# Performance work log

Hardware: AMD Instinct MI355X
Metric: run time of the kernel (lower is better)

## Reference

```python
import jax, jax.numpy as jnp
import numpy as np

B, I, T, H, O = 256, 128, 256, 512, 2
EPS = 1e-5  # BatchNorm1d default eps


def setup_inputs() -> dict:
    key = jax.random.key(0)
    ks = jax.random.split(key, 32)
    stdv = 1.0 / np.sqrt(H)
    u = lambda k, shape: jax.random.uniform(k, shape, jnp.float32, -stdv, stdv)
    X = jax.random.normal(ks[0], (B, I, T), jnp.float32)
    Mask = (jax.random.uniform(ks[1], (B, I, T)) > 0.5).astype(jnp.float32)
    Delta = jax.random.uniform(ks[2], (B, I, T)) * 5.0
    inp = jnp.stack([X, Mask, Delta], axis=1)  # [B, 3, I, T]
    return dict(
        input=inp,
        x_mean=jnp.float32(0.0),
        W_dg_x=u(ks[3], (I, I)), b_dg_x=u(ks[4], (I,)),
        W_dg_h=u(ks[5], (I, H)), b_dg_h=u(ks[6], (H,)),
        W_xz=u(ks[7], (I, H)), W_hz=u(ks[8], (H, H)), W_mz=u(ks[9], (I, H)), b_z=u(ks[10], (H,)),
        W_xr=u(ks[11], (I, H)), W_hr=u(ks[12], (H, H)), W_mr=u(ks[13], (I, H)), b_r=u(ks[14], (H,)),
        W_xh=u(ks[15], (I, H)), W_hh=u(ks[16], (H, H)), W_mh=u(ks[17], (I, H)), b_h=u(ks[18], (H,)),
        W_hy=u(ks[19], (H, O)), b_hy=u(ks[20], (O,)),
        bn_gamma=u(ks[21], (H,)), bn_beta=u(ks[22], (H,)),
    )


def reference(input, x_mean, W_dg_x, b_dg_x, W_dg_h, b_dg_h,
              W_xz, W_hz, W_mz, b_z, W_xr, W_hr, W_mr, b_r,
              W_xh, W_hh, W_mh, b_h, W_hy, b_hy, bn_gamma, bn_beta):
    # input: [B, 3, I, T] -> time-major [T, B, I]
    Xs = jnp.transpose(input[:, 0], (2, 0, 1))
    Ms = jnp.transpose(input[:, 1], (2, 0, 1))
    Ds = jnp.transpose(input[:, 2], (2, 0, 1))
    b, i = input.shape[0], input.shape[2]
    h0 = jnp.zeros((b, W_hz.shape[0]), input.dtype)       # Hidden_State buffer (zeros, broadcast over batch)
    xl0 = jnp.zeros((b, i), input.dtype)                   # X_last_obs buffer

    def step(carry, xs):
        h, x_last = carry
        x, m, d = xs
        gamma_x = jnp.exp(-jax.nn.relu(d @ W_dg_x + b_dg_x))   # [B, I]
        gamma_h = jnp.exp(-jax.nn.relu(d @ W_dg_h + b_dg_h))   # [B, H]
        x_last = jnp.where(m > 0, x, x_last)
        x = m * x + (1 - m) * (gamma_x * x_last + (1 - gamma_x) * x_mean)
        h = gamma_h * h
        z = jax.nn.sigmoid(x @ W_xz + h @ W_hz + m @ W_mz + b_z)
        r = jax.nn.sigmoid(x @ W_xr + h @ W_hr + m @ W_mr + b_r)
        h_tilde = jnp.tanh(x @ W_xh + (r * h) @ W_hh + m @ W_mh + b_h)
        h = (1 - z) * h + z * h_tilde
        # BatchNorm1d in training mode: batch mean, biased variance
        mu = h.mean(axis=0)
        var = ((h - mu) ** 2).mean(axis=0)
        h = bn_gamma * (h - mu) * jax.lax.rsqrt(var + EPS) + bn_beta
        y = jax.nn.softplus(h @ W_hy + b_hy)
        return (h, x_last), (y, h)

    _, (ys, hs) = jax.lax.scan(step, (h0, xl0), (Xs, Ms, Ds))
    # back to batch-major [B, T, *]
    return jnp.transpose(ys, (1, 0, 2)), jnp.transpose(hs, (1, 0, 2))
```

## Files before the change

kernel.cpp:

```cpp
#include <hip/hip_runtime.h>
#include <math.h>

#define Bb 256
#define Ii 128
#define Tt 256
#define Hh 512
#define Oo 2
#define TBr (Tt*Bb)
#define EPS_BN 1e-5f

typedef __attribute__((ext_vector_type(8))) short short8;
typedef __attribute__((ext_vector_type(8))) __bf16 bf16x8;
typedef __attribute__((ext_vector_type(4))) float f32x4;
typedef unsigned long long u64;

__device__ __forceinline__ f32x4 mfma_bf16(short8 a, short8 b, f32x4 c) {
    return __builtin_amdgcn_mfma_f32_16x16x32_bf16(
        __builtin_bit_cast(bf16x8, a), __builtin_bit_cast(bf16x8, b), c, 0, 0, 0);
}
__device__ __forceinline__ short f2bf(float f) {
    union { float f; unsigned u; } v; v.f = f;
    unsigned r = (v.u + 0x7FFFu + ((v.u >> 16) & 1u)) >> 16;
    return (short)r;
}
__device__ __forceinline__ float bf2f(short s) {
    union { unsigned u; float f; } v; v.u = ((unsigned)(unsigned short)s) << 16;
    return v.f;
}
__device__ __forceinline__ float sigmoidf_(float x) { return 1.f / (1.f + expf(-x)); }
__device__ __forceinline__ float softplusf_(float x) { return fmaxf(x, 0.f) + log1pf(expf(-fabsf(x))); }

#define ALD_F(p)  __hip_atomic_load((p),  __ATOMIC_RELAXED, __HIP_MEMORY_SCOPE_AGENT)
#define AST_F(p,v) __hip_atomic_store((p), (v), __ATOMIC_RELAXED, __HIP_MEMORY_SCOPE_AGENT)
#define AADD_F(p,v) (void)__hip_atomic_fetch_add((p), (v), __ATOMIC_RELAXED, __HIP_MEMORY_SCOPE_AGENT)

__device__ __forceinline__ short8 ald16(const short* p) {
    union { u64 u[2]; short8 s; } v;
    v.u[0] = ALD_F((const u64*)p);
    v.u[1] = ALD_F((const u64*)(p + 4));
    return v.s;
}
__device__ __forceinline__ u64 pack4bf(float a, float b, float c_, float d) {
    return (u64)(unsigned short)f2bf(a)
         | ((u64)(unsigned short)f2bf(b) << 16)
         | ((u64)(unsigned short)f2bf(c_) << 32)
         | ((u64)(unsigned short)f2bf(d) << 48);
}

__global__ __launch_bounds__(1024) void repack_kernel(const float* __restrict__ in,
                                                      float* __restrict__ Xall,
                                                      short* __restrict__ Mall,
                                                      short* __restrict__ Dall)
{
    __shared__ float tile[32][33];
    const int bz = blockIdx.z;
    const int b = bz / 3, cch = bz % 3;
    const int t0 = blockIdx.x * 32, i0 = blockIdx.y * 32;
    const int tx = threadIdx.x, ty = threadIdx.y;
    const float* src = in + ((size_t)b * 3 + cch) * (size_t)Ii * Tt;
    tile[ty][tx] = src[(size_t)(i0 + ty) * Tt + t0 + tx];
    __syncthreads();
    const float v = tile[tx][ty];
    const size_t off = ((size_t)(t0 + ty) * Bb + b) * Ii + i0 + tx;
    if (cch == 0)      Xall[off] = v;
    else if (cch == 1) Mall[off] = f2bf(v);
    else               Dall[off] = f2bf(v);
}

__global__ __launch_bounds__(256) void pack_weights_kernel(
    const float* __restrict__ W_dg_x, const float* __restrict__ W_dg_h,
    const float* __restrict__ W_xz, const float* __restrict__ W_hz, const float* __restrict__ W_mz, const float* __restrict__ b_z,
    const float* __restrict__ W_xr, const float* __restrict__ W_hr, const float* __restrict__ W_mr, const float* __restrict__ b_r,
    const float* __restrict__ W_xh, const float* __restrict__ W_hh, const float* __restrict__ W_mh,
    short* __restrict__ Wc1T, short* __restrict__ Wc2T,
    short* __restrict__ WdgxT, short* __restrict__ WdghT, float* __restrict__ bias1)
{
    const int idx = blockIdx.x * blockDim.x + threadIdx.x;
    const int n1 = 1024 * 768, n2 = 512 * 768, n3 = 128 * 128, n4 = 512 * 128;
    if (idx < n1) {
        const int n = idx / 768, k = idx % 768;
        const int col = (n < Hh) ? n : (n - Hh);
        const float* Wx = (n < Hh) ? W_xz : W_xr;
        const float* Wm = (n < Hh) ? W_mz : W_mr;
        const float* Wh = (n < Hh) ? W_hz : W_hr;
        float v;
        if (k < Ii)        v = Wx[(size_t)k * Hh + col];
        else if (k < 2*Ii) v = Wm[(size_t)(k - Ii) * Hh + col];
        else               v = Wh[(size_t)(k - 2*Ii) * Hh + col];
        Wc1T[idx] = f2bf(v);
    } else if (idx < n1 + n2) {
        const int j = idx - n1;
        const int n = j / 768, k = j % 768;
        float v;
        if (k < Ii)        v = W_xh[(size_t)k * Hh + n];
        else if (k < 2*Ii) v = W_mh[(size_t)(k - Ii) * Hh + n];
        else               v = W_hh[(size_t)(k - 2*Ii) * Hh + n];
        Wc2T[j] = f2bf(v);
    } else if (idx < n1 + n2 + n3) {
        const int j = idx - n1 - n2;
        const int n = j >> 7, k = j & 127;
        WdgxT[j] = f2bf(W_dg_x[(size_t)k * Ii + n]);
    } else if (idx < n1 + n2 + n3 + n4) {
        const int j = idx - n1 - n2 - n3;
        const int n = j >> 7, k = j & 127;
        WdghT[j] = f2bf(W_dg_h[(size_t)k * Hh + n]);
    } else if (idx < n1 + n2 + n3 + n4 + 1024) {
        const int n = idx - n1 - n2 - n3 - n4;
        bias1[n] = (n < Hh) ? b_z[n] : b_r[n - Hh];
    }
}

__global__ __launch_bounds__(64) void gdecay_kernel(const short* __restrict__ A,
                                                    const short* __restrict__ BT,
                                                    const float* __restrict__ bias,
                                                    short* __restrict__ C, int N)
{
    const int lane = threadIdx.x;
    const int c = lane & 15, g = lane >> 4;
    const int m0 = blockIdx.x * 32, n0 = blockIdx.y * 64;
    const short* a0 = A + (size_t)(m0 + c) * Ii + 8 * g;
    const short* a1 = a0 + (size_t)16 * Ii;
    const short* bw = BT + (size_t)(n0 + c) * Ii + 8 * g;
    f32x4 acc[2][4];
    #pragma unroll
    for (int i = 0; i < 2; ++i)
        #pragma unroll
        for (int f = 0; f < 4; ++f) acc[i][f] = (f32x4){0.f, 0.f, 0.f, 0.f};
    #pragma unroll
    for (int k0 = 0; k0 < 128; k0 += 32) {
        const short8 av0 = *(const short8*)(a0 + k0);
        const short8 av1 = *(const short8*)(a1 + k0);
        #pragma unroll
        for (int fn = 0; fn < 4; ++fn) {
            const short8 bv = *(const short8*)(bw + (size_t)fn * 16 * Ii + k0);
            acc[0][fn] = mfma_bf16(av0, bv, acc[0][fn]);
            acc[1][fn] = mfma_bf16(av1, bv, acc[1][fn]);
        }
    }
    #pragma unroll
    for (int fn = 0; fn < 4; ++fn) {
        const int n = n0 + fn * 16 + c;
        const float bs = bias[n];
        #pragma unroll
        for (int fm = 0; fm < 2; ++fm) {
            #pragma unroll
            for (int j = 0; j < 4; ++j) {
                const int m = m0 + fm * 16 + 4 * g + j;
                const float v = expf(-fmaxf(acc[fm][fn][j] + bs, 0.f));
                C[(size_t)m * N + n] = f2bf(v);
            }
        }
    }
}

__global__ __launch_bounds__(256) void xeff_scan_kernel(const float* __restrict__ Xall,
                                                        const short* __restrict__ Mall,
                                                        const short* __restrict__ Gx,
                                                        const float* __restrict__ xmean_p,
                                                        short* __restrict__ Xe)
{
    const int bi = blockIdx.x * blockDim.x + threadIdx.x;
    if (bi >= Bb * Ii) return;
    const float xm = xmean_p[0];
    float xl = 0.f;
    for (int t = 0; t < Tt; ++t) {
        const size_t off = (size_t)t * Bb * Ii + bi;
        const float x = Xall[off];
        const float m = bf2f(Mall[off]);
        const float gx = bf2f(Gx[off]);
        if (m > 0.f) xl = x;
        Xe[off] = f2bf(m * x + (1.f - m) * (gx * xl + (1.f - gx) * xm));
    }
}

#define XM_STR 264
#define HP_STR 520
#define GH_STR 520

__global__ __launch_bounds__(512, 1) void grud_persistent(
    const short* __restrict__ Xe, const short* __restrict__ Ma,
    const short* __restrict__ Ghb,
    const short* __restrict__ Wc1T, const short* __restrict__ Wc2T,
    const float* __restrict__ bias1, const float* __restrict__ b_h,
    const float* __restrict__ bn_g, const float* __restrict__ bn_b,
    const float* __restrict__ Why, const float* __restrict__ bhy,
    short* __restrict__ rhG,
    short* __restrict__ HrawG,
    float* __restrict__ PstSum,
    int* __restrict__ f1,
    int* __restrict__ f2,
    float* __restrict__ out_hs, float* __restrict__ out_ys)
{
    const int bid = blockIdx.x, tid = threadIdx.x;
    const int w = tid >> 6, lane = tid & 63, c = lane & 15, g = lane >> 4;
    const int mt = bid & 15, ng = bid >> 4;
    const int m0 = mt * 16;

    __shared__ short sXM[16 * XM_STR];
    __shared__ short sHP[16 * HP_STR];
    __shared__ short sGH[16 * GH_STR];
    __shared__ float sZ[32 * 17];
    __shared__ float scratch[1536];
    __shared__ float sWhy[1024];
    __shared__ float scs[512], shs[512];
    __shared__ float ysred[16];

    sWhy[tid] = Why[tid]; sWhy[tid + 512] = Why[tid + 512];
    const float bhy0 = bhy[0], bhy1 = bhy[1];

    const int colt = w & 3, kh = w >> 2;
    const int colbaseA = (colt < 2) ? (ng * 32 + colt * 16)
                                    : (512 + ng * 32 + (colt - 2) * 16);
    short8 wA[12];
    {
        const short* bw = Wc1T + (size_t)(colbaseA + c) * 768 + kh * 384 + 8 * g;
        #pragma unroll
        for (int s = 0; s < 12; ++s) wA[s] = *(const short8*)(bw + 32 * s);
    }
    const int colt2 = w & 1, kq = w >> 1;
    const int colbaseB = ng * 32 + colt2 * 16;
    short8 wB[6];
    {
        const short* bw = Wc2T + (size_t)(colbaseB + c) * 768 + kq * 192 + 8 * g;
        #pragma unroll
        for (int s = 0; s < 6; ++s) wB[s] = *(const short8*)(bw + 32 * s);
    }
    const int npeer = (kq == 1) ? 4 : (kq >= 2 ? 6 : 0);
    const int peer0 = (kq == 1) ? 0 : (kq == 2 ? 4 : 10);
    const int peerflag = (lane < npeer) ? ((mt + 16 * (peer0 + lane)) * 16) : -1;

    {
        const int r = tid >> 5, cu = tid & 31;
        const short* src = (cu < 16)
            ? (Xe + ((size_t)(m0 + r)) * Ii + 8 * cu)
            : (Ma + ((size_t)(m0 + r)) * Ii + 8 * (cu - 16));
        *(short8*)(&sXM[r * XM_STR + 8 * cu]) = *(const short8*)src;
    }
    __syncthreads();

    float hkeep[16];

    for (int t = 0; t < Tt; ++t) {
        f32x4 accA = (f32x4){0.f, 0.f, 0.f, 0.f};
        f32x4 accB = (f32x4){0.f, 0.f, 0.f, 0.f};
        if (kh == 0) {
            #pragma unroll
            for (int s = 0; s < 8; ++s)
                accA = mfma_bf16(wA[s],
                    *(const short8*)(&sXM[c * XM_STR + 32 * s + 8 * g]), accA);
        }
        #pragma unroll
        for (int s = 0; s < 6; ++s) {
            const int k = kq * 192 + 32 * s;
            if (k < 256)
                accB = mfma_bf16(wB[s],
                    *(const short8*)(&sXM[c * XM_STR + k + 8 * g]), accB);
        }

        if (t > 0) {
            const int pR = (t + 2) % 3;
            u64 hvu[4];
            #pragma unroll
            for (int i = 0; i < 4; ++i) {
                const int idx = tid + i * 512;
                const int r = idx >> 7, c4 = (idx & 127) * 4;
                hvu[i] = ALD_F((const u64*)(HrawG + (size_t)(m0 + r) * Hh + c4));
            }
            const float s1 = ALD_F(&PstSum[pR * 1024 + tid]);
            const float s2 = ALD_F(&PstSum[pR * 1024 + 512 + tid]);
            {
                const float mu = s1 * (1.f / 256.f);
                const float var = fmaxf(s2 * (1.f / 256.f) - mu * mu, 0.f);
                const float sc = bn_g[tid] * rsqrtf(var + EPS_BN);
                scs[tid] = sc; shs[tid] = bn_b[tid] - mu * sc;
            }
            __syncthreads();
            #pragma unroll
            for (int i = 0; i < 4; ++i) {
                const int idx = tid + i * 512;
                const int r = idx >> 7, c4 = (idx & 127) * 4;
                union { u64 u; unsigned short us[4]; } hv, gv;
                hv.u = hvu[i];
                gv.u = *(const u64*)(&sGH[r * GH_STR + c4]);
                float h[4];
                #pragma unroll
                for (int j = 0; j < 4; ++j) {
                    h[j] = fmaf(bf2f((short)hv.us[j]), scs[c4 + j], shs[c4 + j]);
                    hkeep[i * 4 + j] = h[j];
                }
                *(u64*)(&sHP[r * HP_STR + c4]) =
                    pack4bf(h[0] * bf2f((short)gv.us[0]), h[1] * bf2f((short)gv.us[1]),
                            h[2] * bf2f((short)gv.us[2]), h[3] * bf2f((short)gv.us[3]));
            }
            __syncthreads();
        } else {
            #pragma unroll
            for (int i = 0; i < 4; ++i) {
                const int idx = tid + i * 512;
                const int r = idx >> 7, c4 = (idx & 127) * 4;
                *(u64*)(&sHP[r * HP_STR + c4]) = 0ull;
            }
            __syncthreads();
        }

        if (kh == 0) {
            #pragma unroll
            for (int s = 8; s < 12; ++s)
                accA = mfma_bf16(wA[s],
                    *(const short8*)(&sHP[c * HP_STR + (32 * s - 256) + 8 * g]), accA);
        } else {
            #pragma unroll
            for (int s = 0; s < 12; ++s)
                accA = mfma_bf16(wA[s],
                    *(const short8*)(&sHP[c * HP_STR + 128 + 32 * s + 8 * g]), accA);
        }
        if (kh == 1) {
            float* sp = scratch + (colt * 64 + lane) * 4;
            sp[0] = accA[0]; sp[1] = accA[1]; sp[2] = accA[2]; sp[3] = accA[3];
        }
        __syncthreads();
        if (kh == 0) {
            const float* sp = scratch + (colt * 64 + lane) * 4;
            accA[0] += sp[0]; accA[1] += sp[1]; accA[2] += sp[2]; accA[3] += sp[3];
            if (colt < 2) {
                #pragma unroll
                for (int j = 0; j < 4; ++j) {
                    const int lc = colt * 16 + 4 * g + j;
                    const float v = sigmoidf_(accA[j] + bias1[ng * 32 + lc]);
                    sZ[lc * 17 + c] = v;
                }
            } else {
                const int nn0 = ng * 32 + (colt - 2) * 16 + 4 * g;
                float rv[4];
                #pragma unroll
                for (int j = 0; j < 4; ++j) {
                    const float v = sigmoidf_(accA[j] + bias1[512 + nn0 + j]);
                    rv[j] = v * bf2f(sHP[c * HP_STR + nn0 + j]);
                }
                AST_F((u64*)(rhG + ((size_t)(m0 + c) * Hh + nn0)),
                      pack4bf(rv[0], rv[1], rv[2], rv[3]));
            }
        }
        __syncthreads();
        if (tid == 0) AST_F(&f1[bid * 16], t + 1);
        if (t > 0) {
            float p0 = 0.f, p1 = 0.f;
            #pragma unroll
            for (int i = 0; i < 4; ++i) {
                const int idx = tid + i * 512;
                const int r = idx >> 7, c4 = (idx & 127) * 4;
                if ((c4 >> 5) == ng) {
                    *(f32x4*)(&out_hs[((size_t)(m0 + r) * Tt + (t - 1)) * Hh + c4]) =
                        (f32x4){hkeep[i*4+0], hkeep[i*4+1], hkeep[i*4+2], hkeep[i*4+3]};
                }
                if (r == ng) {
                    #pragma unroll
                    for (int j = 0; j < 4; ++j) {
                        p0 = fmaf(hkeep[i*4+j], sWhy[2 * (c4 + j)], p0);
                        p1 = fmaf(hkeep[i*4+j], sWhy[2 * (c4 + j) + 1], p1);
                    }
                }
            }
            #pragma unroll
            for (int s = 1; s < 64; s <<= 1) { p0 += __shfl_xor(p0, s); p1 += __shfl_xor(p1, s); }
            if (lane == 0) { ysred[2 * w] = p0; ysred[2 * w + 1] = p1; }
        }
        if (t + 1 < Tt) {
            #pragma unroll
            for (int i = 0; i < 4; ++i) {
                const int idx = tid + i * 512;
                const int r = idx >> 7, c4 = (idx & 127) * 4;
                const u64 v = *(const u64*)(Ghb + ((size_t)(t + 1) * Bb + m0 + r) * Hh + c4);
                *(u64*)(&sGH[r * GH_STR + c4]) = v;
            }
        }
        if (tid < 4) AST_F(&PstSum[((t + 1) % 3) * 1024 + bid * 4 + tid], 0.f);
        if (t > 0) {
            __syncthreads();
            if (tid == 0) {
                float q0 = 0.f, q1 = 0.f;
                #pragma unroll
                for (int i = 0; i < 8; ++i) { q0 += ysred[2 * i]; q1 += ysred[2 * i + 1]; }
                out_ys[((size_t)(m0 + ng) * Tt + (t - 1)) * Oo + 0] = softplusf_(q0 + bhy0);
                out_ys[((size_t)(m0 + ng) * Tt + (t - 1)) * Oo + 1] = softplusf_(q1 + bhy1);
            }
        }

        if (npeer > 0) {
            for (;;) {
                const int v = (lane < npeer)
                    ? __hip_atomic_load(&f1[peerflag], __ATOMIC_RELAXED, __HIP_MEMORY_SCOPE_AGENT)
                    : 0x7fffffff;
                if (__all(v >= t + 1)) break;
                __builtin_amdgcn_s_sleep(1);
            }
            asm volatile("" ::: "memory");
        }
        #pragma unroll
        for (int s = 0; s < 6; ++s) {
            const int k = kq * 192 + 32 * s;
            if (k >= 256)
                accB = mfma_bf16(wB[s],
                    ald16(rhG + (size_t)(m0 + c) * Hh + (k - 256) + 8 * g), accB);
        }
        if (kq > 0) {
            float* sp = scratch + ((colt2 * 3 + kq - 1) * 64 + lane) * 4;
            sp[0] = accB[0]; sp[1] = accB[1]; sp[2] = accB[2]; sp[3] = accB[3];
        }
        __syncthreads();
        if (kq == 0) {
            #pragma unroll
            for (int qq = 0; qq < 3; ++qq) {
                const float* sp = scratch + ((colt2 * 3 + qq) * 64 + lane) * 4;
                accB[0] += sp[0]; accB[1] += sp[1]; accB[2] += sp[2]; accB[3] += sp[3];
            }
            const int pC = t % 3;
            float hr4[4];
            #pragma unroll
            for (int j = 0; j < 4; ++j) {
                const int lc = colt2 * 16 + 4 * g + j;
                const int col = ng * 32 + lc;
                const float pre = accB[j] + b_h[col];
                const float z = sZ[lc * 17 + c];
                const float hp = bf2f(sHP[c * HP_STR + col]);
                hr4[j] = (1.f - z) * hp + z * tanhf(pre);
            }
            const int cb = ng * 32 + colt2 * 16 + 4 * g;
            AST_F((u64*)(HrawG + (size_t)(m0 + c) * Hh + cb),
                  pack4bf(hr4[0], hr4[1], hr4[2], hr4[3]));
            #pragma unroll
            for (int j = 0; j < 4; ++j) {
                float sp_ = hr4[j], sq_ = hr4[j] * hr4[j];
                sp_ += __shfl_xor(sp_, 1); sq_ += __shfl_xor(sq_, 1);
                sp_ += __shfl_xor(sp_, 2); sq_ += __shfl_xor(sq_, 2);
                sp_ += __shfl_xor(sp_, 4); sq_ += __shfl_xor(sq_, 4);
                sp_ += __shfl_xor(sp_, 8); sq_ += __shfl_xor(sq_, 8);
                if (c == 0) {
                    const int col = ng * 32 + colt2 * 16 + 4 * g + j;
                    AADD_F(&PstSum[pC * 1024 + col], sp_);
                    AADD_F(&PstSum[pC * 1024 + 512 + col], sq_);
                }
            }
        }
        __syncthreads();
        if (tid == 0) AST_F(&f2[bid * 16], t + 1);
        if (t + 1 < Tt) {
            const int r = tid >> 5, cu = tid & 31;
            const short* src = (cu < 16)
                ? (Xe + ((size_t)(t + 1) * Bb + m0 + r) * Ii + 8 * cu)
                : (Ma + ((size_t)(t + 1) * Bb + m0 + r) * Ii + 8 * (cu - 16));
            *(short8*)(&sXM[r * XM_STR + 8 * cu]) = *(const short8*)src;
        }
        if (tid < 64) {
            for (;;) {
                const int v0 = __hip_atomic_load(&f2[(tid * 4 + 0) * 16], __ATOMIC_RELAXED, __HIP_MEMORY_SCOPE_AGENT);
                const int v1 = __hip_atomic_load(&f2[(tid * 4 + 1) * 16], __ATOMIC_RELAXED, __HIP_MEMORY_SCOPE_AGENT);
                const int v2 = __hip_atomic_load(&f2[(tid * 4 + 2) * 16], __ATOMIC_RELAXED, __HIP_MEMORY_SCOPE_AGENT);
                const int v3 = __hip_atomic_load(&f2[(tid * 4 + 3) * 16], __ATOMIC_RELAXED, __HIP_MEMORY_SCOPE_AGENT);
                int mn = v0 < v1 ? v0 : v1;
                mn = mn < v2 ? mn : v2;
                mn = mn < v3 ? mn : v3;
                if (__all(mn >= t + 1)) break;
                __builtin_amdgcn_s_sleep(1);
            }
        }
        __syncthreads();
    }

    {
        const int pR = (Tt - 1) % 3;
        {
            const float s1 = ALD_F(&PstSum[pR * 1024 + tid]);
            const float s2 = ALD_F(&PstSum[pR * 1024 + 512 + tid]);
            const float mu = s1 * (1.f / 256.f);
            const float var = fmaxf(s2 * (1.f / 256.f) - mu * mu, 0.f);
            const float sc = bn_g[tid] * rsqrtf(var + EPS_BN);
            scs[tid] = sc; shs[tid] = bn_b[tid] - mu * sc;
        }
        __syncthreads();
        float p0 = 0.f, p1 = 0.f;
        #pragma unroll
        for (int i = 0; i < 4; ++i) {
            const int idx = tid + i * 512;
            const int r = idx >> 7, c4 = (idx & 127) * 4;
            union { u64 u; unsigned short us[4]; } hv;
            hv.u = ALD_F((const u64*)(HrawG + (size_t)(m0 + r) * Hh + c4));
            float h[4];
            #pragma unroll
            for (int j = 0; j < 4; ++j)
                h[j] = fmaf(bf2f((short)hv.us[j]), scs[c4 + j], shs[c4 + j]);
            if ((c4 >> 5) == ng) {
                *(f32x4*)(&out_hs[((size_t)(m0 + r) * Tt + (Tt - 1)) * Hh + c4]) =
                    (f32x4){h[0], h[1], h[2], h[3]};
            }
            if (r == ng) {
                #pragma unroll
                for (int j = 0; j < 4; ++j) {
                    p0 = fmaf(h[j], sWhy[2 * (c4 + j)], p0);
                    p1 = fmaf(h[j], sWhy[2 * (c4 + j) + 1], p1);
                }
            }
        }
        #pragma unroll
        for (int s = 1; s < 64; s <<= 1) { p0 += __shfl_xor(p0, s); p1 += __shfl_xor(p1, s); }
        if (lane == 0) { ysred[2 * w] = p0; ysred[2 * w + 1] = p1; }
        __syncthreads();
        if (tid == 0) {
            float q0 = 0.f, q1 = 0.f;
            #pragma unroll
            for (int i = 0; i < 8; ++i) { q0 += ysred[2 * i]; q1 += ysred[2 * i + 1]; }
            out_ys[((size_t)(m0 + ng) * Tt + (Tt - 1)) * Oo + 0] = softplusf_(q0 + bhy0);
            out_ys[((size_t)(m0 + ng) * Tt + (Tt - 1)) * Oo + 1] = softplusf_(q1 + bhy1);
        }
    }
}

extern "C" void kernel_launch(void* const* d_in, const int* in_sizes, int n_in,
                              void* d_out, int out_size, void* d_ws, size_t ws_size,
                              hipStream_t stream)
{
    const float* input  = (const float*)d_in[0];
    const float* xmean  = (const float*)d_in[1];
    const float* W_dg_x = (const float*)d_in[2];
    const float* b_dg_x = (const float*)d_in[3];
    const float* W_dg_h = (const float*)d_in[4];
    const float* b_dg_h = (const float*)d_in[5];
    const float* W_xz   = (const float*)d_in[6];
    const float* W_hz   = (const float*)d_in[7];
    const float* W_mz   = (const float*)d_in[8];
    const float* b_z    = (const float*)d_in[9];
    const float* W_xr   = (const float*)d_in[10];
    const float* W_hr   = (const float*)d_in[11];
    const float* W_mr   = (const float*)d_in[12];
    const float* b_r    = (const float*)d_in[13];
    const float* W_xh   = (const float*)d_in[14];
    const float* W_hh   = (const float*)d_in[15];
    const float* W_mh   = (const float*)d_in[16];
    const float* b_h    = (const float*)d_in[17];
    const float* W_hy   = (const float*)d_in[18];
    const float* b_hy   = (const float*)d_in[19];
    const float* bn_g   = (const float*)d_in[20];
    const float* bn_b   = (const float*)d_in[21];

    float* out_ys = (float*)d_out;
    float* out_hs = out_ys + (size_t)Bb * Tt * Oo;

    char* p = (char*)d_ws;
    float* Xall = (float*)p;            p += (size_t)TBr * Ii * 4;
    short* Mall = (short*)p;            p += (size_t)TBr * Ii * 2;
    short* Dall = (short*)p;            p += (size_t)TBr * Ii * 2;
    short* Gxb  = (short*)p;            p += (size_t)TBr * Ii * 2;
    short* Ghb  = (short*)p;            p += (size_t)TBr * Hh * 2;
    short* Xe   = (short*)p;            p += (size_t)TBr * Ii * 2;
    short* Wc1T = (short*)p;            p += (size_t)1024 * 768 * 2;
    short* Wc2T = (short*)p;            p += (size_t)512 * 768 * 2;
    short* WdgxT= (short*)p;            p += (size_t)128 * 128 * 2;
    short* WdghT= (short*)p;            p += (size_t)512 * 128 * 2;
    float* bias1= (float*)p;            p += 1024 * 4;
    short* rhG  = (short*)p;            p += (size_t)Bb * Hh * 2;
    short* HrawG= (short*)p;            p += (size_t)Bb * Hh * 2;
    float* PstSum=(float*)p;            p += 3 * 1024 * 4;
    int*   f1   = (int*)p;              p += 256 * 16 * 4;
    int*   f2   = (int*)p;              p += 256 * 16 * 4;

    hipMemsetAsync(f1, 0, 256 * 16 * 4, stream);
    hipMemsetAsync(f2, 0, 256 * 16 * 4, stream);
    hipMemsetAsync(PstSum, 0, 3 * 1024 * 4, stream);

    repack_kernel<<<dim3(Tt / 32, Ii / 32, Bb * 3), dim3(32, 32), 0, stream>>>(input, Xall, Mall, Dall);

    {
        const int total = 1024 * 768 + 512 * 768 + 128 * 128 + 512 * 128 + 1024;
        pack_weights_kernel<<<(total + 255) / 256, 256, 0, stream>>>(
            W_dg_x, W_dg_h,
            W_xz, W_hz, W_mz, b_z,
            W_xr, W_hr, W_mr, b_r,
            W_xh, W_hh, W_mh,
            Wc1T, Wc2T, WdgxT, WdghT, bias1);
    }

    gdecay_kernel<<<dim3(TBr / 32, Ii / 64), 64, 0, stream>>>(Dall, WdgxT, b_dg_x, Gxb, Ii);
    gdecay_kernel<<<dim3(TBr / 32, Hh / 64), 64, 0, stream>>>(Dall, WdghT, b_dg_h, Ghb, Hh);

    xeff_scan_kernel<<<(Bb * Ii) / 256, 256, 0, stream>>>(Xall, Mall, Gxb, xmean, Xe);

    grud_persistent<<<256, 512, 0, stream>>>(
        Xe, Mall, Ghb, Wc1T, Wc2T, bias1, b_h, bn_g, bn_b,
        W_hy, b_hy, rhG, HrawG, PstSum, f1, f2, out_hs, out_ys);
}
```

Measured before the change: 2.294 ms.

## Compute BN scale per thread, prefetch h loads early, drop per-step barriers

Each thread now owns a fixed 4-column slice, so it computes the BatchNorm scale and shift for its own columns in registers instead of staging them in shared memory. That removes one __syncthreads per timestep. The global loads of raw h and the partial statistics are issued at the top of the step, before the input MFMAs, so their latency overlaps with compute. The ys reduction is moved after an existing barrier onto a different thread, which drops a second barrier per step. The cost is some redundant rsqrt work, since each column's scale is now computed by four threads, plus extra registers held across the MFMA section.

```diff
diff --git a/kernel.cpp b/kernel.cpp
--- a/kernel.cpp
+++ b/kernel.cpp
@@ -202,10 +202,11 @@
     __shared__ float sZ[32 * 17];
     __shared__ float scratch[1536];
     __shared__ float sWhy[1024];
-    __shared__ float scs[512], shs[512];
+    __shared__ float sBg[512], sBb[512];
     __shared__ float ysred[16];
 
     sWhy[tid] = Why[tid]; sWhy[tid + 512] = Why[tid + 512];
+    sBg[tid] = bn_g[tid]; sBb[tid] = bn_b[tid];
     const float bhy0 = bhy[0], bhy1 = bhy[1];
 
     const int colt = w & 3, kh = w >> 2;
@@ -229,6 +230,10 @@
     const int peer0 = (kq == 1) ? 0 : (kq == 2 ? 4 : 10);
     const int peerflag = (lane < npeer) ? ((mt + 16 * (peer0 + lane)) * 16) : -1;
 
+    const int c4s = (tid & 127) * 4;
+    const int rb0 = tid >> 7;
+    const bool myng = (c4s >> 5) == ng;
+
     {
         const int r = tid >> 5, cu = tid & 31;
         const short* src = (cu < 16)
@@ -241,6 +246,19 @@
     float hkeep[16];
 
     for (int t = 0; t < Tt; ++t) {
+        u64 hvu[4];
+        u64 s1a = 0, s1b = 0, s2a = 0, s2b = 0;
+        if (t > 0) {
+            const int pR = (t + 2) % 3;
+            #pragma unroll
+            for (int i = 0; i < 4; ++i)
+                hvu[i] = ALD_F((const u64*)(HrawG + (size_t)(m0 + rb0 + 4 * i) * Hh + c4s));
+            s1a = ALD_F((const u64*)&PstSum[pR * 1024 + c4s]);
+            s1b = ALD_F((const u64*)&PstSum[pR * 1024 + c4s + 2]);
+            s2a = ALD_F((const u64*)&PstSum[pR * 1024 + 512 + c4s]);
+            s2b = ALD_F((const u64*)&PstSum[pR * 1024 + 512 + c4s + 2]);
+        }
+
         f32x4 accA = (f32x4){0.f, 0.f, 0.f, 0.f};
         f32x4 accB = (f32x4){0.f, 0.f, 0.f, 0.f};
         if (kh == 0) {
@@ -258,50 +276,44 @@
         }
 
         if (t > 0) {
-            const int pR = (t + 2) % 3;
-            u64 hvu[4];
+            union { u64 u; float f[2]; } ua, ub;
+            float sc4[4], sh4[4];
+            {
+                float sum4[4], sq4[4];
+                ua.u = s1a; ub.u = s1b;
+                sum4[0] = ua.f[0]; sum4[1] = ua.f[1]; sum4[2] = ub.f[0]; sum4[3] = ub.f[1];
+                ua.u = s2a; ub.u = s2b;
+                sq4[0] = ua.f[0]; sq4[1] = ua.f[1]; sq4[2] = ub.f[0]; sq4[3] = ub.f[1];
+                #pragma unroll
+                for (int j = 0; j < 4; ++j) {
+                    const float mu = sum4[j] * (1.f / 256.f);
+                    const float var = fmaxf(sq4[j] * (1.f / 256.f) - mu * mu, 0.f);
+                    const float sc = sBg[c4s + j] * rsqrtf(var + EPS_BN);
+                    sc4[j] = sc; sh4[j] = sBb[c4s + j] - mu * sc;
+                }
+            }
             #pragma unroll
             for (int i = 0; i < 4; ++i) {
-                const int idx = tid + i * 512;
-                const int r = idx >> 7, c4 = (idx & 127) * 4;
-                hvu[i] = ALD_F((const u64*)(HrawG + (size_t)(m0 + r) * Hh + c4));
-            }
-            const float s1 = ALD_F(&PstSum[pR * 1024 + tid]);
-            const float s2 = ALD_F(&PstSum[pR * 1024 + 512 + tid]);
-            {
-                const float mu = s1 * (1.f / 256.f);
-                const float var = fmaxf(s2 * (1.f / 256.f) - mu * mu, 0.f);
-                const float sc = bn_g[tid] * rsqrtf(var + EPS_BN);
-                scs[tid] = sc; shs[tid] = bn_b[tid] - mu * sc;
-            }
-            __syncthreads();
-            #pragma unroll
-            for (int i = 0; i < 4; ++i) {
-                const int idx = tid + i * 512;
-                const int r = idx >> 7, c4 = (idx & 127) * 4;
+                const int r = rb0 + 4 * i;
                 union { u64 u; unsigned short us[4]; } hv, gv;
                 hv.u = hvu[i];
-                gv.u = *(const u64*)(&sGH[r * GH_STR + c4]);
+                gv.u = *(const u64*)(&sGH[r * GH_STR + c4s]);
                 float h[4];
                 #pragma unroll
                 for (int j = 0; j < 4; ++j) {
-                    h[j] = fmaf(bf2f((short)hv.us[j]), scs[c4 + j], shs[c4 + j]);
+                    h[j] = fmaf(bf2f((short)hv.us[j]), sc4[j], sh4[j]);
                     hkeep[i * 4 + j] = h[j];
                 }
-                *(u64*)(&sHP[r * HP_STR + c4]) =
+                *(u64*)(&sHP[r * HP_STR + c4s]) =
                     pack4bf(h[0] * bf2f((short)gv.us[0]), h[1] * bf2f((short)gv.us[1]),
                             h[2] * bf2f((short)gv.us[2]), h[3] * bf2f((short)gv.us[3]));
             }
-            __syncthreads();
         } else {
             #pragma unroll
-            for (int i = 0; i < 4; ++i) {
-                const int idx = tid + i * 512;
-                const int r = idx >> 7, c4 = (idx & 127) * 4;
-                *(u64*)(&sHP[r * HP_STR + c4]) = 0ull;
-            }
-            __syncthreads();
-        }
+            for (int i = 0; i < 4; ++i)
+                *(u64*)(&sHP[(rb0 + 4 * i) * HP_STR + c4s]) = 0ull;
+        }
+        __syncthreads();
 
         if (kh == 0) {
             #pragma unroll
@@ -347,17 +359,16 @@
             float p0 = 0.f, p1 = 0.f;
             #pragma unroll
             for (int i = 0; i < 4; ++i) {
-                const int idx = tid + i * 512;
-                const int r = idx >> 7, c4 = (idx & 127) * 4;
-                if ((c4 >> 5) == ng) {
-                    *(f32x4*)(&out_hs[((size_t)(m0 + r) * Tt + (t - 1)) * Hh + c4]) =
+                const int r = rb0 + 4 * i;
+                if (myng) {
+                    *(f32x4*)(&out_hs[((size_t)(m0 + r) * Tt + (t - 1)) * Hh + c4s]) =
                         (f32x4){hkeep[i*4+0], hkeep[i*4+1], hkeep[i*4+2], hkeep[i*4+3]};
                 }
                 if (r == ng) {
                     #pragma unroll
                     for (int j = 0; j < 4; ++j) {
-                        p0 = fmaf(hkeep[i*4+j], sWhy[2 * (c4 + j)], p0);
-                        p1 = fmaf(hkeep[i*4+j], sWhy[2 * (c4 + j) + 1], p1);
+                        p0 = fmaf(hkeep[i*4+j], sWhy[2 * (c4s + j)], p0);
+                        p1 = fmaf(hkeep[i*4+j], sWhy[2 * (c4s + j) + 1], p1);
                     }
                 }
             }
@@ -368,23 +379,12 @@
         if (t + 1 < Tt) {
             #pragma unroll
             for (int i = 0; i < 4; ++i) {
-                const int idx = tid + i * 512;
-                const int r = idx >> 7, c4 = (idx & 127) * 4;
-                const u64 v = *(const u64*)(Ghb + ((size_t)(t + 1) * Bb + m0 + r) * Hh + c4);
-                *(u64*)(&sGH[r * GH_STR + c4]) = v;
+                const int r = rb0 + 4 * i;
+                const u64 v = *(const u64*)(Ghb + ((size_t)(t + 1) * Bb + m0 + r) * Hh + c4s);
+                *(u64*)(&sGH[r * GH_STR + c4s]) = v;
             }
         }
         if (tid < 4) AST_F(&PstSum[((t + 1) % 3) * 1024 + bid * 4 + tid], 0.f);
-        if (t > 0) {
-            __syncthreads();
-            if (tid == 0) {
-                float q0 = 0.f, q1 = 0.f;
-                #pragma unroll
-                for (int i = 0; i < 8; ++i) { q0 += ysred[2 * i]; q1 += ysred[2 * i + 1]; }
-                out_ys[((size_t)(m0 + ng) * Tt + (t - 1)) * Oo + 0] = softplusf_(q0 + bhy0);
-                out_ys[((size_t)(m0 + ng) * Tt + (t - 1)) * Oo + 1] = softplusf_(q1 + bhy1);
-            }
-        }
 
         if (npeer > 0) {
             for (;;) {
@@ -408,6 +408,13 @@
             sp[0] = accB[0]; sp[1] = accB[1]; sp[2] = accB[2]; sp[3] = accB[3];
         }
         __syncthreads();
+        if (t > 0 && tid == 256) {
+            float q0 = 0.f, q1 = 0.f;
+            #pragma unroll
+            for (int i = 0; i < 8; ++i) { q0 += ysred[2 * i]; q1 += ysred[2 * i + 1]; }
+            out_ys[((size_t)(m0 + ng) * Tt + (t - 1)) * Oo + 0] = softplusf_(q0 + bhy0);
+            out_ys[((size_t)(m0 + ng) * Tt + (t - 1)) * Oo + 1] = softplusf_(q1 + bhy1);
+        }
         if (kq == 0) {
             #pragma unroll
             for (int qq = 0; qq < 3; ++qq) {
@@ -469,35 +476,43 @@
 
     {
         const int pR = (Tt - 1) % 3;
+        float sc4[4], sh4[4];
         {
-            const float s1 = ALD_F(&PstSum[pR * 1024 + tid]);
-            const float s2 = ALD_F(&PstSum[pR * 1024 + 512 + tid]);
-            const float mu = s1 * (1.f / 256.f);
-            const float var = fmaxf(s2 * (1.f / 256.f) - mu * mu, 0.f);
-            const float sc = bn_g[tid] * rsqrtf(var + EPS_BN);
-            scs[tid] = sc; shs[tid] = bn_b[tid] - mu * sc;
-        }
-        __syncthreads();
+            union { u64 u; float f[2]; } ua, ub;
+            float sum4[4], sq4[4];
+            ua.u = ALD_F((const u64*)&PstSum[pR * 1024 + c4s]);
+            ub.u = ALD_F((const u64*)&PstSum[pR * 1024 + c4s + 2]);
+            sum4[0] = ua.f[0]; sum4[1] = ua.f[1]; sum4[2] = ub.f[0]; sum4[3] = ub.f[1];
+            ua.u = ALD_F((const u64*)&PstSum[pR * 1024 + 512 + c4s]);
+            ub.u = ALD_F((const u64*)&PstSum[pR * 1024 + 512 + c4s + 2]);
+            sq4[0] = ua.f[0]; sq4[1] = ua.f[1]; sq4[2] = ub.f[0]; sq4[3] = ub.f[1];
+            #pragma unroll
+            for (int j = 0; j < 4; ++j) {
+                const float mu = sum4[j] * (1.f / 256.f);
+                const float var = fmaxf(sq4[j] * (1.f / 256.f) - mu * mu, 0.f);
+                const float sc = sBg[c4s + j] * rsqrtf(var + EPS_BN);
+                sc4[j] = sc; sh4[j] = sBb[c4s + j] - mu * sc;
+            }
+        }
         float p0 = 0.f, p1 = 0.f;
         #pragma unroll
         for (int i = 0; i < 4; ++i) {
-            const int idx = tid + i * 512;
-            const int r = idx >> 7, c4 = (idx & 127) * 4;
+            const int r = rb0 + 4 * i;
             union { u64 u; unsigned short us[4]; } hv;
-            hv.u = ALD_F((const u64*)(HrawG + (size_t)(m0 + r) * Hh + c4));
+            hv.u = ALD_F((const u64*)(HrawG + (size_t)(m0 + r) * Hh + c4s));
             float h[4];
             #pragma unroll
             for (int j = 0; j < 4; ++j)
-                h[j] = fmaf(bf2f((short)hv.us[j]), scs[c4 + j], shs[c4 + j]);
-            if ((c4 >> 5) == ng) {
-                *(f32x4*)(&out_hs[((size_t)(m0 + r) * Tt + (Tt - 1)) * Hh + c4]) =
+                h[j] = fmaf(bf2f((short)hv.us[j]), sc4[j], sh4[j]);
+            if (myng) {
+                *(f32x4*)(&out_hs[((size_t)(m0 + r) * Tt + (Tt - 1)) * Hh + c4s]) =
                     (f32x4){h[0], h[1], h[2], h[3]};
             }
             if (r == ng) {
                 #pragma unroll
                 for (int j = 0; j < 4; ++j) {
-                    p0 = fmaf(h[j], sWhy[2 * (c4 + j)], p0);
-                    p1 = fmaf(h[j], sWhy[2 * (c4 + j) + 1], p1);
+                    p0 = fmaf(h[j], sWhy[2 * (c4s + j)], p0);
+                    p1 = fmaf(h[j], sWhy[2 * (c4s + j) + 1], p1);
                 }
             }
         }
```

Result: faster. 2.246 ms (-2.1%).
